# Kernel tuning notes

Hardware: AMD Instinct MI355X
Metric: run time of the kernel (lower is better)

The kernel has to match this reference:

```python
import jax, jax.numpy as jnp
import numpy as np

GRID_H, GRID_W, BOX, CLASSES = 13, 13, 5, 80
COORD_FACTOR, NO_OBJECT_FACTOR, OBJECT_FACTOR, CLASS_FACTOR = 1.0, 1.0, 5.0, 1.0
ANCHORS = jnp.array([0.57273, 0.677385, 1.87446, 2.06253, 3.33843, 5.47434,
                     7.88282, 3.52778, 9.77052, 9.16828], dtype=jnp.float32)


def setup_inputs() -> dict:
    key = jax.random.key(0)
    k1, k2, k3 = jax.random.split(key, 3)
    B, T = 256, 50
    y_true = jax.random.uniform(k1, (B, GRID_H, GRID_W, BOX, 5 + CLASSES), dtype=jnp.float32)
    y_pred = jax.random.normal(k2, (B, GRID_H, GRID_W, BOX, 5 + CLASSES), dtype=jnp.float32)
    true_boxes = jax.random.uniform(k3, (B, 1, 1, 1, T, 4), dtype=jnp.float32)
    return {"y_true": y_true, "y_pred": y_pred, "true_boxes": true_boxes}


def reference(y_true, y_pred, true_boxes):
    f32 = jnp.float32
    anchors = ANCHORS.reshape(1, 1, 1, BOX, 2)
    # cell grid exactly as in torch: tile(range(13), 13).reshape(1,13,13,1,1)
    cell_w = jnp.tile(jnp.arange(GRID_H, dtype=f32), (GRID_W,)).reshape(1, GRID_H, GRID_W, 1, 1)
    cell_h = jnp.transpose(cell_w, (0, 2, 1, 3, 4))
    cell_grid = jnp.concatenate([cell_w, cell_h], axis=-1)  # [1,13,13,1,2]

    pred_box_xy = jax.nn.sigmoid(y_pred[..., :2]) + cell_grid          # [B,13,13,5,2]
    pred_box_wh = jnp.exp(y_pred[..., 2:4]) * anchors                  # [B,13,13,5,2]
    pred_box_conf = jax.nn.sigmoid(y_pred[..., 4])                      # [B,13,13,5]
    pred_box_class = y_pred[..., 5:]                                    # [B,13,13,5,80]

    true_box_xy = y_true[..., 0:2]
    true_box_wh = y_true[..., 2:4]

    # IoU between pred and matched true box per anchor cell
    t_half = true_box_wh / 2.0
    t_mins, t_maxes = true_box_xy - t_half, true_box_xy + t_half
    p_half = pred_box_wh / 2.0
    p_mins, p_maxes = pred_box_xy - p_half, pred_box_xy + p_half
    i_wh = jnp.maximum(jnp.minimum(p_maxes, t_maxes) - jnp.maximum(p_mins, t_mins), 0.0)
    i_areas = i_wh[..., 0] * i_wh[..., 1]
    union = pred_box_wh[..., 0] * pred_box_wh[..., 1] + true_box_wh[..., 0] * true_box_wh[..., 1] - i_areas
    iou = i_areas / union
    true_box_conf = iou * y_true[..., 4]
    true_box_class = jnp.argmax(y_true[..., 5:], axis=-1)               # [B,13,13,5]

    coord_mask = y_true[..., 4:5] * COORD_FACTOR                        # [B,13,13,5,1]

    # broadcast IoU vs all true boxes -> [B,13,13,5,T]
    tb_xy, tb_wh = true_boxes[..., 0:2], true_boxes[..., 2:4]
    tb_half = tb_wh / 2.0
    tb_mins, tb_maxes = tb_xy - tb_half, tb_xy + tb_half
    pxy = pred_box_xy[:, :, :, :, None, :]                               # [B,13,13,5,1,2]
    pwh = pred_box_wh[:, :, :, :, None, :]
    pw_half = pwh / 2.0
    pb_mins, pb_maxes = pxy - pw_half, pxy + pw_half
    bi_wh = jnp.maximum(jnp.minimum(pb_maxes, tb_maxes) - jnp.maximum(pb_mins, tb_mins), 0.0)
    bi_areas = bi_wh[..., 1] * bi_wh[..., 0]
    b_union = pwh[..., 0] * pwh[..., 1] + tb_wh[..., 0] * tb_wh[..., 1] - bi_areas
    best_ious = jnp.max(bi_areas / b_union, axis=4)                      # [B,13,13,5]

    conf_mask = (best_ious < 0.6).astype(f32) * (1.0 - y_true[..., 4]) * NO_OBJECT_FACTOR
    conf_mask = conf_mask + true_box_conf * OBJECT_FACTOR
    class_mask = y_true[..., 4] * CLASS_FACTOR

    nb_coord = jnp.sum((coord_mask > 0.0).astype(f32))
    nb_conf = jnp.sum((conf_mask > 0.0).astype(f32))
    nb_class = jnp.sum((class_mask > 0.0).astype(f32))

    loss_xy = jnp.sum(jnp.square(true_box_xy - pred_box_xy) * coord_mask) / (nb_coord + 1e-6) / 2.0
    loss_wh = jnp.sum(jnp.square(true_box_wh - pred_box_wh) * coord_mask) / (nb_coord + 1e-6) / 2.0
    loss_conf = jnp.sum(jnp.square(true_box_conf - pred_box_conf) * conf_mask) / (nb_conf + 1e-6) / 2.0

    logp = jax.nn.log_softmax(pred_box_class, axis=-1)                   # [B,13,13,5,80]
    ce = -jnp.take_along_axis(logp, true_box_class[..., None], axis=-1)[..., 0]
    loss_class = jnp.sum(ce * class_mask) / (nb_class + 1e-6)

    return loss_xy + loss_wh + loss_conf + loss_class
```

## Files before the change

### kernel.cpp

```cpp
#include <hip/hip_runtime.h>
#include <math.h>

#define GRID_HW   13
#define NBOX      5
#define NCLASS    80
#define REC       85
#define CPB_CELLS (GRID_HW*GRID_HW*NBOX)
#define T_BOXES   50
#define THREADS   256
#define QPB       (THREADS/4)

__device__ __constant__ float c_anchors[10] = {
    0.57273f, 0.677385f, 1.87446f, 2.06253f, 3.33843f,
    5.47434f, 7.88282f, 3.52778f, 9.77052f, 9.16828f};

template <int USE_ATOMIC>
__global__ __launch_bounds__(THREADS, 6)
void yolo_loss_main(const float* __restrict__ y_true,
                    const float* __restrict__ y_pred,
                    const float* __restrict__ tboxes,
                    double* __restrict__ partials,
                    int n_cells)
{
    __shared__ double red[4][8];

    const int tid  = threadIdx.x;
    const int q    = tid & 3;
    const int quad = tid >> 2;
    const int cell = blockIdx.x * QPB + quad;

    double p_xy = 0.0, p_wh = 0.0, p_conf = 0.0, p_ce = 0.0;
    double p_nc = 0.0, p_nf = 0.0, p_ncl = 0.0;

    if (cell < n_cells) {
        int b    = cell / CPB_CELLS;
        int rem  = cell - b * CPB_CELLS;
        int h    = rem / (GRID_HW * NBOX);
        int rem2 = rem - h * (GRID_HW * NBOX);
        int w    = rem2 / NBOX;
        int box  = rem2 - w * NBOX;

        const float* __restrict__ yt = y_true + (size_t)cell * REC;
        const float* __restrict__ yp = y_pred + (size_t)cell * REC;

        const float tx = yt[0], ty = yt[1], tw = yt[2], th = yt[3], yt4 = yt[4];
        const float r0 = yp[0], r1 = yp[1], r2 = yp[2], r3 = yp[3], r4 = yp[4];

        const float px = 1.f / (1.f + expf(-r0)) + (float)w;
        const float py = 1.f / (1.f + expf(-r1)) + (float)h;
        const float pw = expf(r2) * c_anchors[2 * box];
        const float ph = expf(r3) * c_anchors[2 * box + 1];
        const float pconf = 1.f / (1.f + expf(-r4));

        const float pw2 = pw * 0.5f, ph2 = ph * 0.5f;
        const float p_minx = px - pw2, p_maxx = px + pw2;
        const float p_miny = py - ph2, p_maxy = py + ph2;

        float tw2 = tw * 0.5f, th2 = th * 0.5f;
        float iw = fmaxf(fminf(p_maxx, tx + tw2) - fmaxf(p_minx, tx - tw2), 0.f);
        float ih = fmaxf(fminf(p_maxy, ty + th2) - fmaxf(p_miny, ty - th2), 0.f);
        float inter = iw * ih;
        float iou = inter / (pw * ph + tw * th - inter);
        const float true_conf = iou * yt4;

        float amax = -INFINITY; int aidx = 0x7fffffff;
        float lmax = -INFINITY;
        #pragma unroll
        for (int k = 0; k < NCLASS / 4; ++k) {
            int c = q + 4 * k;
            float tv = yt[5 + c];
            float pv = yp[5 + c];
            if (tv > amax) { amax = tv; aidx = c; }
            lmax = fmaxf(lmax, pv);
        }
        #pragma unroll
        for (int m = 1; m <= 2; m <<= 1) {
            float ov = __shfl_xor(amax, m);
            int   oi = __shfl_xor(aidx, m);
            if (ov > amax || (ov == amax && oi < aidx)) { amax = ov; aidx = oi; }
            lmax = fmaxf(lmax, __shfl_xor(lmax, m));
        }

        float lsum = 0.f;
        #pragma unroll
        for (int k = 0; k < NCLASS / 4; ++k)
            lsum += expf(yp[5 + q + 4 * k] - lmax);
        #pragma unroll
        for (int m = 1; m <= 2; m <<= 1)
            lsum += __shfl_xor(lsum, m);
        const float ce = -(yp[5 + aidx] - lmax - logf(lsum));

        const float4* tb = (const float4*)(tboxes + (size_t)b * T_BOXES * 4);
        float best = -INFINITY;
        #pragma unroll 2
        for (int t = q; t < T_BOXES; t += 4) {
            float4 bx = tb[t];
            float bw2 = bx.z * 0.5f, bh2 = bx.w * 0.5f;
            float iw2 = fmaxf(fminf(p_maxx, bx.x + bw2) - fmaxf(p_minx, bx.x - bw2), 0.f);
            float ih2 = fmaxf(fminf(p_maxy, bx.y + bh2) - fmaxf(p_miny, bx.y - bh2), 0.f);
            float ia = iw2 * ih2;
            float r  = ia / (pw * ph + bx.z * bx.w - ia);
            best = fmaxf(best, r);
        }
        #pragma unroll
        for (int m = 1; m <= 2; m <<= 1)
            best = fmaxf(best, __shfl_xor(best, m));

        if (q == 0) {
            const float cm = yt4;
            p_xy = (double)(((tx - px) * (tx - px) + (ty - py) * (ty - py)) * cm);
            p_wh = (double)(((tw - pw) * (tw - pw) + (th - ph) * (th - ph)) * cm);
            float conf_mask = ((best < 0.6f) ? 1.f : 0.f) * (1.f - yt4)
                            + true_conf * 5.f;
            p_conf = (double)((true_conf - pconf) * (true_conf - pconf) * conf_mask);
            p_ce   = (double)(ce * yt4);
            p_nc   = (cm > 0.f)        ? 1.0 : 0.0;
            p_nf   = (conf_mask > 0.f) ? 1.0 : 0.0;
            p_ncl  = (yt4 > 0.f)       ? 1.0 : 0.0;
        }
    }

    double v[7] = {p_xy, p_wh, p_conf, p_ce, p_nc, p_nf, p_ncl};
    #pragma unroll
    for (int k = 0; k < 7; ++k) {
        #pragma unroll
        for (int off = 32; off > 0; off >>= 1)
            v[k] += __shfl_down(v[k], off);
    }
    const int wave = tid >> 6, lane = tid & 63;
    if (lane == 0) {
        #pragma unroll
        for (int k = 0; k < 7; ++k) red[wave][k] = v[k];
    }
    __syncthreads();
    if (tid < 8) {
        double s = (tid < 7) ? (red[0][tid] + red[1][tid] + red[2][tid] + red[3][tid])
                             : 0.0;
        if (USE_ATOMIC) {
            if (tid < 7) unsafeAtomicAdd(&partials[tid], s);
        } else {
            partials[(size_t)blockIdx.x * 8 + tid] = s;
        }
    }
}

template <int USE_ATOMIC>
__global__ __launch_bounds__(1024)
void yolo_loss_final(const double* __restrict__ partials,
                     float* __restrict__ out, int nblocks)
{
    __shared__ double red[16][8];
    const int tid = threadIdx.x;

    if (USE_ATOMIC) {
        if (tid == 0) {
            double nbc  = partials[4] + 1e-6;
            double nbf  = partials[5] + 1e-6;
            double nbcl = partials[6] + 1e-6;
            out[0] = (float)(partials[0] / nbc * 0.5 + partials[1] / nbc * 0.5 +
                             partials[2] / nbf * 0.5 + partials[3] / nbcl);
        }
        return;
    }

    double v[7] = {0, 0, 0, 0, 0, 0, 0};
    for (int i = tid; i < nblocks; i += 1024) {
        const double4* p = (const double4*)(partials + (size_t)i * 8);
        double4 a = p[0];
        double4 b = p[1];
        v[0] += a.x; v[1] += a.y; v[2] += a.z; v[3] += a.w;
        v[4] += b.x; v[5] += b.y; v[6] += b.z;
    }
    #pragma unroll
    for (int k = 0; k < 7; ++k) {
        #pragma unroll
        for (int off = 32; off > 0; off >>= 1)
            v[k] += __shfl_down(v[k], off);
    }
    const int wave = tid >> 6, lane = tid & 63;
    if (lane == 0) {
        #pragma unroll
        for (int k = 0; k < 7; ++k) red[wave][k] = v[k];
    }
    __syncthreads();
    if (tid == 0) {
        double s[7];
        #pragma unroll
        for (int k = 0; k < 7; ++k) {
            double acc = 0.0;
            #pragma unroll
            for (int wv = 0; wv < 16; ++wv) acc += red[wv][k];
            s[k] = acc;
        }
        double nbc  = s[4] + 1e-6;
        double nbf  = s[5] + 1e-6;
        double nbcl = s[6] + 1e-6;
        out[0] = (float)(s[0] / nbc * 0.5 + s[1] / nbc * 0.5 +
                         s[2] / nbf * 0.5 + s[3] / nbcl);
    }
}

extern "C" void kernel_launch(void* const* d_in, const int* in_sizes, int n_in,
                              void* d_out, int out_size, void* d_ws, size_t ws_size,
                              hipStream_t stream)
{
    const float* y_true = (const float*)d_in[0];
    const float* y_pred = (const float*)d_in[1];
    const float* tboxes = (const float*)d_in[2];
    float* out  = (float*)d_out;
    double* ws  = (double*)d_ws;

    const int n_cells = in_sizes[0] / REC;
    const int blocks  = (n_cells + QPB - 1) / QPB;
    const size_t need = (size_t)blocks * 8 * sizeof(double);

    if (ws_size >= need) {
        yolo_loss_main<0><<<blocks, THREADS, 0, stream>>>(y_true, y_pred, tboxes, ws, n_cells);
        yolo_loss_final<0><<<1, 1024, 0, stream>>>(ws, out, blocks);
    } else {
        hipMemsetAsync(d_ws, 0, 7 * sizeof(double), stream);
        yolo_loss_main<1><<<blocks, THREADS, 0, stream>>>(y_true, y_pred, tboxes, ws, n_cells);
        yolo_loss_final<1><<<1, 64, 0, stream>>>(ws, out, blocks);
    }
}
```

Baseline: 183.4 us.

## Stage cell tiles through LDS with coalesced float4 loads in grid-stride loop

Each block now loads 32 cells of y_true and y_pred into shared memory with coalesced float4 loads, then processes them with 16 lanes per cell instead of 4. A persistent grid-stride loop capped at a maximum grid size accumulates per-thread partials across tiles. The goal is to replace strided, uncoalesced per-cell global loads (85-float records) with coalesced bulk loads and to cut the number of block partials. The cost is extra LDS traffic and barriers per tile, along with higher register and LDS pressure from the 512-thread blocks.

```diff
diff --git a/kernel.cpp b/kernel.cpp
--- a/kernel.cpp
+++ b/kernel.cpp
@@ -7,125 +7,162 @@
 #define REC       85
 #define CPB_CELLS (GRID_HW*GRID_HW*NBOX)
 #define T_BOXES   50
-#define THREADS   256
-#define QPB       (THREADS/4)
+#define THREADS   512
+#define CPT       32
+#define LPC       16
+#define TILE_FLOATS (CPT*REC)
+#define TILE_F4     (TILE_FLOATS/4)
+#define MAX_GRID  3380
 
 __device__ __constant__ float c_anchors[10] = {
     0.57273f, 0.677385f, 1.87446f, 2.06253f, 3.33843f,
     5.47434f, 7.88282f, 3.52778f, 9.77052f, 9.16828f};
 
 template <int USE_ATOMIC>
-__global__ __launch_bounds__(THREADS, 6)
+__global__ __launch_bounds__(THREADS, 8)
 void yolo_loss_main(const float* __restrict__ y_true,
                     const float* __restrict__ y_pred,
                     const float* __restrict__ tboxes,
                     double* __restrict__ partials,
-                    int n_cells)
+                    int n_cells, int ntiles)
 {
-    __shared__ double red[4][8];
-
-    const int tid  = threadIdx.x;
-    const int q    = tid & 3;
-    const int quad = tid >> 2;
-    const int cell = blockIdx.x * QPB + quad;
+    __shared__ float4 lbuf4[2 * TILE_F4];
+    __shared__ double red[8][8];
+
+    float* const lt = (float*)lbuf4;
+    float* const lp = lt + TILE_FLOATS;
+
+    const int tid = threadIdx.x;
+    const int g   = tid & (LPC - 1);
+    const int cl  = tid >> 4;
 
     double p_xy = 0.0, p_wh = 0.0, p_conf = 0.0, p_ce = 0.0;
     double p_nc = 0.0, p_nf = 0.0, p_ncl = 0.0;
 
-    if (cell < n_cells) {
-        int b    = cell / CPB_CELLS;
-        int rem  = cell - b * CPB_CELLS;
-        int h    = rem / (GRID_HW * NBOX);
-        int rem2 = rem - h * (GRID_HW * NBOX);
-        int w    = rem2 / NBOX;
-        int box  = rem2 - w * NBOX;
-
-        const float* __restrict__ yt = y_true + (size_t)cell * REC;
-        const float* __restrict__ yp = y_pred + (size_t)cell * REC;
-
-        const float tx = yt[0], ty = yt[1], tw = yt[2], th = yt[3], yt4 = yt[4];
-        const float r0 = yp[0], r1 = yp[1], r2 = yp[2], r3 = yp[3], r4 = yp[4];
-
-        const float px = 1.f / (1.f + expf(-r0)) + (float)w;
-        const float py = 1.f / (1.f + expf(-r1)) + (float)h;
-        const float pw = expf(r2) * c_anchors[2 * box];
-        const float ph = expf(r3) * c_anchors[2 * box + 1];
-        const float pconf = 1.f / (1.f + expf(-r4));
-
-        const float pw2 = pw * 0.5f, ph2 = ph * 0.5f;
-        const float p_minx = px - pw2, p_maxx = px + pw2;
-        const float p_miny = py - ph2, p_maxy = py + ph2;
-
-        float tw2 = tw * 0.5f, th2 = th * 0.5f;
-        float iw = fmaxf(fminf(p_maxx, tx + tw2) - fmaxf(p_minx, tx - tw2), 0.f);
-        float ih = fmaxf(fminf(p_maxy, ty + th2) - fmaxf(p_miny, ty - th2), 0.f);
-        float inter = iw * ih;
-        float iou = inter / (pw * ph + tw * th - inter);
-        const float true_conf = iou * yt4;
-
-        float amax = -INFINITY; int aidx = 0x7fffffff;
-        float lmax = -INFINITY;
-        #pragma unroll
-        for (int k = 0; k < NCLASS / 4; ++k) {
-            int c = q + 4 * k;
-            float tv = yt[5 + c];
-            float pv = yp[5 + c];
-            if (tv > amax) { amax = tv; aidx = c; }
-            lmax = fmaxf(lmax, pv);
-        }
-        #pragma unroll
-        for (int m = 1; m <= 2; m <<= 1) {
-            float ov = __shfl_xor(amax, m);
-            int   oi = __shfl_xor(aidx, m);
-            if (ov > amax || (ov == amax && oi < aidx)) { amax = ov; aidx = oi; }
-            lmax = fmaxf(lmax, __shfl_xor(lmax, m));
-        }
-
-        float lsum = 0.f;
-        #pragma unroll
-        for (int k = 0; k < NCLASS / 4; ++k)
-            lsum += expf(yp[5 + q + 4 * k] - lmax);
-        #pragma unroll
-        for (int m = 1; m <= 2; m <<= 1)
-            lsum += __shfl_xor(lsum, m);
-        const float ce = -(yp[5 + aidx] - lmax - logf(lsum));
-
-        const float4* tb = (const float4*)(tboxes + (size_t)b * T_BOXES * 4);
-        float best = -INFINITY;
-        #pragma unroll 2
-        for (int t = q; t < T_BOXES; t += 4) {
-            float4 bx = tb[t];
-            float bw2 = bx.z * 0.5f, bh2 = bx.w * 0.5f;
-            float iw2 = fmaxf(fminf(p_maxx, bx.x + bw2) - fmaxf(p_minx, bx.x - bw2), 0.f);
-            float ih2 = fmaxf(fminf(p_maxy, bx.y + bh2) - fmaxf(p_miny, bx.y - bh2), 0.f);
-            float ia = iw2 * ih2;
-            float r  = ia / (pw * ph + bx.z * bx.w - ia);
-            best = fmaxf(best, r);
-        }
-        #pragma unroll
-        for (int m = 1; m <= 2; m <<= 1)
-            best = fmaxf(best, __shfl_xor(best, m));
-
-        if (q == 0) {
-            const float cm = yt4;
-            p_xy = (double)(((tx - px) * (tx - px) + (ty - py) * (ty - py)) * cm);
-            p_wh = (double)(((tw - pw) * (tw - pw) + (th - ph) * (th - ph)) * cm);
-            float conf_mask = ((best < 0.6f) ? 1.f : 0.f) * (1.f - yt4)
-                            + true_conf * 5.f;
-            p_conf = (double)((true_conf - pconf) * (true_conf - pconf) * conf_mask);
-            p_ce   = (double)(ce * yt4);
-            p_nc   = (cm > 0.f)        ? 1.0 : 0.0;
-            p_nf   = (conf_mask > 0.f) ? 1.0 : 0.0;
-            p_ncl  = (yt4 > 0.f)       ? 1.0 : 0.0;
+    for (int tile = blockIdx.x; tile < ntiles; tile += gridDim.x) {
+        __syncthreads();
+
+        const int cellbase = tile * CPT;
+        const int remc = min(CPT, n_cells - cellbase);
+        if (remc == CPT) {
+            const float4* __restrict__ gt4 = (const float4*)(y_true + (size_t)cellbase * REC);
+            const float4* __restrict__ gp4 = (const float4*)(y_pred + (size_t)cellbase * REC);
+            #pragma unroll
+            for (int r = 0; r < 3; ++r) {
+                const int idx = r * THREADS + tid;
+                if (idx < 2 * TILE_F4)
+                    lbuf4[idx] = (idx < TILE_F4) ? gt4[idx] : gp4[idx - TILE_F4];
+            }
+        } else {
+            const int nf = remc * REC;
+            const size_t base = (size_t)cellbase * REC;
+            for (int i = tid; i < nf; i += THREADS) {
+                lt[i] = y_true[base + i];
+                lp[i] = y_pred[base + i];
+            }
+        }
+        __syncthreads();
+
+        const int cell = cellbase + cl;
+        if (cell < n_cells) {
+            int b    = cell / CPB_CELLS;
+            int rem  = cell - b * CPB_CELLS;
+            int h    = rem / (GRID_HW * NBOX);
+            int rem2 = rem - h * (GRID_HW * NBOX);
+            int w    = rem2 / NBOX;
+            int box  = rem2 - w * NBOX;
+
+            const float* __restrict__ yt = lt + cl * REC;
+            const float* __restrict__ yp = lp + cl * REC;
+
+            const float tx = yt[0], ty = yt[1], tw = yt[2], th = yt[3], yt4 = yt[4];
+            const float r0 = yp[0], r1 = yp[1], r2 = yp[2], r3 = yp[3], r4 = yp[4];
+
+            const float px = 1.f / (1.f + expf(-r0)) + (float)w;
+            const float py = 1.f / (1.f + expf(-r1)) + (float)h;
+            const float pw = expf(r2) * c_anchors[2 * box];
+            const float ph = expf(r3) * c_anchors[2 * box + 1];
+            const float pconf = 1.f / (1.f + expf(-r4));
+
+            const float pw2 = pw * 0.5f, ph2 = ph * 0.5f;
+            const float p_minx = px - pw2, p_maxx = px + pw2;
+            const float p_miny = py - ph2, p_maxy = py + ph2;
+
+            float tw2 = tw * 0.5f, th2 = th * 0.5f;
+            float iw = fmaxf(fminf(p_maxx, tx + tw2) - fmaxf(p_minx, tx - tw2), 0.f);
+            float ih = fmaxf(fminf(p_maxy, ty + th2) - fmaxf(p_miny, ty - th2), 0.f);
+            float inter = iw * ih;
+            float iou = inter / (pw * ph + tw * th - inter);
+            const float true_conf = iou * yt4;
+
+            float pv[5];
+            float amax = -INFINITY; int aidx = 0x7fffffff;
+            float lmax = -INFINITY;
+            #pragma unroll
+            for (int k = 0; k < 5; ++k) {
+                const int c = 5 * g + k;
+                const float tv  = yt[5 + c];
+                const float pvk = yp[5 + c];
+                pv[k] = pvk;
+                if (tv > amax) { amax = tv; aidx = c; }
+                lmax = fmaxf(lmax, pvk);
+            }
+            #pragma unroll
+            for (int m = 1; m <= 8; m <<= 1) {
+                float ov = __shfl_xor(amax, m);
+                int   oi = __shfl_xor(aidx, m);
+                if (ov > amax || (ov == amax && oi < aidx)) { amax = ov; aidx = oi; }
+                lmax = fmaxf(lmax, __shfl_xor(lmax, m));
+            }
+
+            float lsum = 0.f;
+            #pragma unroll
+            for (int k = 0; k < 5; ++k) lsum += expf(pv[k] - lmax);
+            #pragma unroll
+            for (int m = 1; m <= 8; m <<= 1) lsum += __shfl_xor(lsum, m);
+
+            const float sel = yp[5 + aidx];
+            const float ce  = -(sel - lmax - logf(lsum));
+
+            const float4* __restrict__ tb = (const float4*)(tboxes + (size_t)b * T_BOXES * 4);
+            float best = -INFINITY;
+            #pragma unroll
+            for (int k2 = 0; k2 < 4; ++k2) {
+                const int t = g + LPC * k2;
+                if (t < T_BOXES) {
+                    float4 bx = tb[t];
+                    float bw2 = bx.z * 0.5f, bh2 = bx.w * 0.5f;
+                    float iw2 = fmaxf(fminf(p_maxx, bx.x + bw2) - fmaxf(p_minx, bx.x - bw2), 0.f);
+                    float ih2 = fmaxf(fminf(p_maxy, bx.y + bh2) - fmaxf(p_miny, bx.y - bh2), 0.f);
+                    float ia = iw2 * ih2;
+                    float r  = ia / (pw * ph + bx.z * bx.w - ia);
+                    best = fmaxf(best, r);
+                }
+            }
+            #pragma unroll
+            for (int m = 1; m <= 8; m <<= 1)
+                best = fmaxf(best, __shfl_xor(best, m));
+
+            if (g == 0) {
+                const float cm = yt4;
+                p_xy += (double)(((tx - px) * (tx - px) + (ty - py) * (ty - py)) * cm);
+                p_wh += (double)(((tw - pw) * (tw - pw) + (th - ph) * (th - ph)) * cm);
+                float conf_mask = ((best < 0.6f) ? 1.f : 0.f) * (1.f - yt4)
+                                + true_conf * 5.f;
+                p_conf += (double)((true_conf - pconf) * (true_conf - pconf) * conf_mask);
+                p_ce   += (double)(ce * yt4);
+                p_nc   += (cm > 0.f)        ? 1.0 : 0.0;
+                p_nf   += (conf_mask > 0.f) ? 1.0 : 0.0;
+                p_ncl  += (yt4 > 0.f)       ? 1.0 : 0.0;
+            }
         }
     }
 
     double v[7] = {p_xy, p_wh, p_conf, p_ce, p_nc, p_nf, p_ncl};
     #pragma unroll
     for (int k = 0; k < 7; ++k) {
-        #pragma unroll
-        for (int off = 32; off > 0; off >>= 1)
-            v[k] += __shfl_down(v[k], off);
+        v[k] += __shfl_xor(v[k], 16);
+        v[k] += __shfl_xor(v[k], 32);
     }
     const int wave = tid >> 6, lane = tid & 63;
     if (lane == 0) {
@@ -134,8 +171,11 @@
     }
     __syncthreads();
     if (tid < 8) {
-        double s = (tid < 7) ? (red[0][tid] + red[1][tid] + red[2][tid] + red[3][tid])
-                             : 0.0;
+        double s = 0.0;
+        if (tid < 7) {
+            #pragma unroll
+            for (int wv = 0; wv < 8; ++wv) s += red[wv][tid];
+        }
         if (USE_ATOMIC) {
             if (tid < 7) unsafeAtomicAdd(&partials[tid], s);
         } else {
@@ -211,15 +251,18 @@
     double* ws  = (double*)d_ws;
 
     const int n_cells = in_sizes[0] / REC;
-    const int blocks  = (n_cells + QPB - 1) / QPB;
-    const size_t need = (size_t)blocks * 8 * sizeof(double);
+    const int ntiles  = (n_cells + CPT - 1) / CPT;
+    const int grid    = ntiles < MAX_GRID ? ntiles : MAX_GRID;
+    const size_t need = (size_t)grid * 8 * sizeof(double);
 
     if (ws_size >= need) {
-        yolo_loss_main<0><<<blocks, THREADS, 0, stream>>>(y_true, y_pred, tboxes, ws, n_cells);
-        yolo_loss_final<0><<<1, 1024, 0, stream>>>(ws, out, blocks);
+        yolo_loss_main<0><<<grid, THREADS, 0, stream>>>(y_true, y_pred, tboxes, ws,
+                                                        n_cells, ntiles);
+        yolo_loss_final<0><<<1, 1024, 0, stream>>>(ws, out, grid);
     } else {
         hipMemsetAsync(d_ws, 0, 7 * sizeof(double), stream);
-        yolo_loss_main<1><<<blocks, THREADS, 0, stream>>>(y_true, y_pred, tboxes, ws, n_cells);
-        yolo_loss_final<1><<<1, 64, 0, stream>>>(ws, out, blocks);
+        yolo_loss_main<1><<<grid, THREADS, 0, stream>>>(y_true, y_pred, tboxes, ws,
+                                                        n_cells, ntiles);
+        yolo_loss_final<1><<<1, 64, 0, stream>>>(ws, out, grid);
     }
 }
```

Measured after the change: 204.9 us. 11.7% more time.
